# Kernel tuning notes

Hardware: AMD Instinct MI355X
Metric: run time of the kernel (lower is better)

The kernel has to match this reference:

```python
import jax, jax.numpy as jnp
import numpy as np

B, C, H, W = 16, 512, 32, 32
NUM_GROUPS = 32
EPS = 1e-5


def setup_inputs() -> dict:
    key = jax.random.key(0)
    ks = jax.random.split(key, 7)
    x = jax.random.normal(ks[0], (B, C, H, W), dtype=jnp.float32)
    gamma = jnp.ones((C,), dtype=jnp.float32)
    beta = jnp.zeros((C,), dtype=jnp.float32)
    # project_in: Conv2d(C, 3C, 1) -> weight [3C, C], bias [3C]
    w_in = jax.random.normal(ks[1], (3 * C, C), dtype=jnp.float32) / np.sqrt(C)
    b_in = jnp.zeros((3 * C,), dtype=jnp.float32)
    # project_out: Conv2d(C, C, 1) with init_scale=0.0 -> zero-init in original;
    # use small random weights so gradients/outputs are non-trivial for testing.
    w_out = jax.random.normal(ks[2], (C, C), dtype=jnp.float32) / np.sqrt(C)
    b_out = jnp.zeros((C,), dtype=jnp.float32)
    return {"x": x, "gamma": gamma, "beta": beta, "w_in": w_in, "b_in": b_in,
            "w_out": w_out, "b_out": b_out}


def group_norm(x, gamma, beta):
    b, c, h, w = x.shape
    xg = x.reshape(b, NUM_GROUPS, c // NUM_GROUPS, h, w)
    mean = xg.mean(axis=(2, 3, 4), keepdims=True)
    var = xg.var(axis=(2, 3, 4), keepdims=True)
    xn = ((xg - mean) * jax.lax.rsqrt(var + EPS)).reshape(b, c, h, w)
    return xn * gamma[None, :, None, None] + beta[None, :, None, None]


def reference(x, gamma, beta, w_in, b_in, w_out, b_out):
    skip = x  # in_channels == out_channels -> Identity skip
    xn = group_norm(x, gamma, beta)
    # 1x1 conv == channel matmul
    qkv = jnp.einsum('oc,bchw->bohw', w_in, xn) + b_in[None, :, None, None]
    q, k, v = jnp.split(qkv, 3, axis=1)  # each [B, C, H, W]
    cm = q.shape[1]
    # [B, H, W, H*W] scores
    scores = jnp.einsum('bchw,bcHW->bhwHW', q, k).reshape(B, H, W, H * W)
    attn = jax.nn.softmax(scores / jnp.sqrt(jnp.float32(cm)), axis=-1)
    attn = attn.reshape(B, H, W, H, W)
    out = jnp.einsum('bhwHW,bcHW->bchw', attn, v)
    out = jnp.einsum('oc,bchw->bohw', w_out, out) + b_out[None, :, None, None]
    return out + skip
```

## Files before the change

### kernel.cpp

```cpp
#include <hip/hip_runtime.h>
#include <hip/hip_bf16.h>
#include <cstdint>
#include <cstddef>

#define HW   1024
#define NC   512
#define NB   16
#define EPSV 1e-5f

typedef __hip_bfloat16 bf16;
typedef __attribute__((ext_vector_type(8))) __bf16 bf16x8;
typedef __attribute__((ext_vector_type(4))) float f32x4;

__device__ __forceinline__ void gload16(const void* g, void* l) {
  __builtin_amdgcn_global_load_lds(
      (const __attribute__((address_space(1))) uint32_t*)g,
      (__attribute__((address_space(3))) uint32_t*)l, 16, 0, 0);
}

__global__ __launch_bounds__(256) void cvt_w_kernel(
    const float* __restrict__ wi, const float* __restrict__ wo,
    bf16* __restrict__ wib, char* __restrict__ wobf) {
  int i = blockIdx.x * 256 + threadIdx.x;
  if (i < 196608) {
    float4 v = ((const float4*)wi)[i];
    union { bf16 h[4]; uint2 u; } p;
    p.h[0] = __float2bfloat16(v.x); p.h[1] = __float2bfloat16(v.y);
    p.h[2] = __float2bfloat16(v.z); p.h[3] = __float2bfloat16(v.w);
    *(uint2*)&wib[(size_t)i * 4] = p.u;
  } else {
    int j = i - 196608;
    float4 v = ((const float4*)wo)[j];
    int elem = j * 4;
    int co = elem >> 9, c = elem & 511;
    union { bf16 h[4]; uint2 u; } p;
    p.h[0] = __float2bfloat16(v.x); p.h[1] = __float2bfloat16(v.y);
    p.h[2] = __float2bfloat16(v.z); p.h[3] = __float2bfloat16(v.w);
    int chh = co >> 4, col_ = co & 15, kc = c >> 5, cc = c & 31;
    *(uint2*)(wobf + (((chh * 16 + kc) << 10) + col_ * 64 + cc * 2)) = p.u;
  }
}

__global__ __launch_bounds__(256) void gn_kernel(
    const float* __restrict__ x, const float* __restrict__ gamma,
    const float* __restrict__ beta, bf16* __restrict__ xn) {
  int blk = blockIdx.x;
  int b = blk >> 5, g = blk & 31;
  size_t base = ((size_t)(b * NC + g * 16)) * HW;
  const float4* src4 = (const float4*)(x + base);
  int t = threadIdx.x;
  float s = 0.f, ss = 0.f;
  float4 v[16];
#pragma unroll
  for (int i = 0; i < 16; ++i) {
    v[i] = src4[t + i * 256];
    s  += v[i].x + v[i].y + v[i].z + v[i].w;
    ss += v[i].x * v[i].x + v[i].y * v[i].y + v[i].z * v[i].z + v[i].w * v[i].w;
  }
  __shared__ float red[256];
  red[t] = s; __syncthreads();
  for (int o = 128; o > 0; o >>= 1) { if (t < o) red[t] += red[t + o]; __syncthreads(); }
  float mean = red[0] * (1.f / 16384.f);
  __syncthreads();
  red[t] = ss; __syncthreads();
  for (int o = 128; o > 0; o >>= 1) { if (t < o) red[t] += red[t + o]; __syncthreads(); }
  float var = red[0] * (1.f / 16384.f) - mean * mean;
  float rstd = rsqrtf(var + EPSV);

  __shared__ bf16 sm[16][1032];
#pragma unroll
  for (int i = 0; i < 16; ++i) {
    int idx = t + i * 256;
    int c = idx >> 8;
    int hw4 = (idx & 255) * 4;
    float gm = gamma[g * 16 + c], bt = beta[g * 16 + c];
    union { bf16 h[4]; uint2 u; } p;
    p.h[0] = __float2bfloat16((v[i].x - mean) * rstd * gm + bt);
    p.h[1] = __float2bfloat16((v[i].y - mean) * rstd * gm + bt);
    p.h[2] = __float2bfloat16((v[i].z - mean) * rstd * gm + bt);
    p.h[3] = __float2bfloat16((v[i].w - mean) * rstd * gm + bt);
    *(uint2*)&sm[c][hw4] = p.u;
  }
  __syncthreads();
  bf16* dst = xn + (size_t)b * HW * NC + g * 16;
#pragma unroll
  for (int it = 0; it < 8; ++it) {
    int u = it * 256 + t;
    int hw = u >> 1;
    int c8 = (u & 1) * 8;
    union { bf16 h[8]; uint4 q; } p;
#pragma unroll
    for (int j = 0; j < 8; ++j) p.h[j] = sm[c8 + j][hw];
    *(uint4*)&dst[(size_t)hw * NC + c8] = p.q;
  }
}

__global__ __launch_bounds__(256) void qkv_gemm(
    const bf16* __restrict__ wib, const bf16* __restrict__ xn,
    const float* __restrict__ bias,
    bf16* __restrict__ qtok, char* __restrict__ kfrag, char* __restrict__ vfrag) {
  __shared__ bf16 sT[2][128][32];
  int z = blockIdx.z;
  const bf16* Bb = xn + (size_t)z * (512 * 1024);
  int n0 = blockIdx.x * 128, m0 = blockIdx.y * 128;
  int t = threadIdx.x;
  int l = t & 63, w = t >> 6;
  int wm = w >> 1, wn = w & 1;

  int srow = t >> 2;
  int scol = (t & 3) * 8;

  f32x4 acc[4][4] = {};

  const bf16* ga0 = wib + (size_t)(m0 + srow) * 512 + scol;
  const bf16* gb0 = Bb + (size_t)(n0 + srow) * 512 + scol;

  for (int k0 = 0; k0 < 512; k0 += 32) {
    gload16(ga0 + k0, &sT[0][srow][scol]);
    gload16(ga0 + (size_t)64 * 512 + k0, &sT[0][64 + srow][scol]);
    gload16(gb0 + k0, &sT[1][srow][scol]);
    gload16(gb0 + (size_t)64 * 512 + k0, &sT[1][64 + srow][scol]);
    __syncthreads();
    bf16x8 af[4], bfr[4];
    int kc = (l >> 4) * 8;
    int ra = wm * 64 + (l & 15);
    int rb = wn * 64 + (l & 15);
#pragma unroll
    for (int i = 0; i < 4; ++i) {
      af[i]  = *(const bf16x8*)&sT[0][ra + i * 16][kc];
      bfr[i] = *(const bf16x8*)&sT[1][rb + i * 16][kc];
    }
#pragma unroll
    for (int i = 0; i < 4; ++i)
#pragma unroll
      for (int j = 0; j < 4; ++j)
        acc[i][j] = __builtin_amdgcn_mfma_f32_16x16x32_bf16(af[i], bfr[j], acc[i][j], 0, 0, 0);
    __syncthreads();
  }

  int rbase = (l >> 4) * 4;
#pragma unroll
  for (int i = 0; i < 4; ++i) {
    int row = m0 + wm * 64 + i * 16 + rbase;
    float4 bv = *(const float4*)&bias[row];
    float bb[4] = {bv.x, bv.y, bv.z, bv.w};
#pragma unroll
    for (int j = 0; j < 4; ++j) {
      int col = n0 + wn * 64 + j * 16 + (l & 15);
      if (m0 < 512) {
        bf16* C = qtok + (size_t)z * 524288;
        union { bf16 h[4]; uint2 u; } p;
#pragma unroll
        for (int r = 0; r < 4; ++r) p.h[r] = __float2bfloat16(acc[i][j][r] + bb[r]);
        *(uint2*)&C[(size_t)col * 512 + row] = p.u;
      } else if (m0 < 1024) {
        char* C = kfrag + (size_t)z * 1048576;
        int rk = row - 512;
        int jflat = col >> 4, j_lo = col & 15;
        int kw = rk >> 5, cc = rk & 31;
        union { bf16 h[4]; uint2 u; } p;
#pragma unroll
        for (int r = 0; r < 4; ++r) p.h[r] = __float2bfloat16(acc[i][j][r] + bb[r]);
        *(uint2*)(C + (((size_t)(jflat * 16 + kw)) << 10) + j_lo * 64 + cc * 2) = p.u;
      } else {
        char* C = vfrag + (size_t)z * 1048576;
        int rv = row - 1024;
        int tile = col >> 7, jj = col & 127;
        int ks = jj >> 5, jc = jj & 31;
#pragma unroll
        for (int r = 0; r < 4; ++r) {
          int ch = rv + r;
          int chh = ch >> 4, chl = ch & 15;
          *(bf16*)(C + (((tile * 32 + chh) * 4 + ks) << 10)
                     + chl * 64 + jc * 2) = __float2bfloat16(acc[i][j][r] + bb[r]);
        }
      }
    }
  }
}

__global__ __launch_bounds__(512, 1) void flash_kernel(
    const bf16* __restrict__ qtok, const bf16* __restrict__ kfrag,
    const bf16* __restrict__ vfrag, const bf16* __restrict__ wfrag,
    const float* __restrict__ b_out, const float* __restrict__ x,
    float* __restrict__ out) {
  __shared__ char lds[98304];
  char* Qs = lds;
  char* Ps = lds + 65536;
  float* redl = (float*)(lds + 65536);

  int id = blockIdx.x;
  int xcd = id & 7, rest = id >> 3;
  int q = rest & 15, bh = rest >> 4;
  int b = xcd + bh * 8;
  int i0 = q * 64;

  const char* qC = (const char*)qtok + (size_t)b * 1048576;
  const char* kC = (const char*)kfrag + (size_t)b * 1048576;
  const char* vC = (const char*)vfrag + (size_t)b * 1048576;
  const char* wC = (const char*)wfrag;

  int t = threadIdx.x, l = t & 63, w = t >> 6;
  int l15 = l & 15, lq = l >> 4;
  int fofs = l15 * 64 + lq * 16;
  int chb = w * 64;

#pragma unroll
  for (int it = 0; it < 8; ++it) {
    int A = it * 8192 + t * 16;
    int ih2 = A >> 14, ks = (A >> 10) & 15, ilo = (A >> 6) & 15, cb = A & 63;
    gload16(qC + (size_t)(i0 + ih2 * 16 + ilo) * 1024 + ks * 64 + cb, Qs + A);
  }

  float lacc[4] = {0.f, 0.f, 0.f, 0.f};
  f32x4 o[4][4] = {};
  const float scl = 0.044194173824159216f;

  __syncthreads();

  for (int tile = 0; tile < 4; ++tile) {
    bf16x8 vfA[4][4];
#pragma unroll
    for (int js = 0; js < 4; ++js)
#pragma unroll
      for (int mi = 0; mi < 4; ++mi) {
        int f = tile * 8 + js;
        vfA[js][mi] = *(const bf16x8*)(vC
            + (((size_t)(((f >> 2) * 32 + (w * 4 + mi)) * 4 + (f & 3))) << 10) + fofs);
      }
    f32x4 s0[4] = {}, s1[4] = {};
#pragma unroll
    for (int kw = 0; kw < 16; ++kw) {
      int jf0 = tile * 16 + w * 2;
      bf16x8 kf0 = *(const bf16x8*)(kC + (((size_t)(jf0 * 16 + kw)) << 10) + fofs);
      bf16x8 kf1 = *(const bf16x8*)(kC + (((size_t)((jf0 + 1) * 16 + kw)) << 10) + fofs);
#pragma unroll
      for (int ni = 0; ni < 4; ++ni) {
        bf16x8 qf = *(const bf16x8*)(Qs + ni * 16384 + kw * 1024 + fofs);
        s0[ni] = __builtin_amdgcn_mfma_f32_16x16x32_bf16(kf0, qf, s0[ni], 0, 0, 0);
        s1[ni] = __builtin_amdgcn_mfma_f32_16x16x32_bf16(kf1, qf, s1[ni], 0, 0, 0);
      }
    }
#pragma unroll
    for (int ni = 0; ni < 4; ++ni) {
#pragma unroll
      for (int jg = 0; jg < 2; ++jg) {
        const f32x4& sv = jg ? s1[ni] : s0[ni];
        float p0 = __expf(sv[0] * scl);
        float p1 = __expf(sv[1] * scl);
        float p2 = __expf(sv[2] * scl);
        float p3 = __expf(sv[3] * scl);
        lacc[ni] += p0 + p1 + p2 + p3;
        union { bf16 h[4]; uint64_t u; } pk;
        pk.h[0] = __float2bfloat16(p0); pk.h[1] = __float2bfloat16(p1);
        pk.h[2] = __float2bfloat16(p2); pk.h[3] = __float2bfloat16(p3);
        *(uint64_t*)(Ps + ni * 8192 + w * 1024 + l15 * 64 + jg * 32 + lq * 8) = pk.u;
      }
    }
    __syncthreads();
    bf16x8 vfB[4][4];
#pragma unroll
    for (int js = 0; js < 4; ++js)
#pragma unroll
      for (int mi = 0; mi < 4; ++mi) {
        int f = tile * 8 + 4 + js;
        vfB[js][mi] = *(const bf16x8*)(vC
            + (((size_t)(((f >> 2) * 32 + (w * 4 + mi)) * 4 + (f & 3))) << 10) + fofs);
      }
#pragma unroll
    for (int js = 0; js < 4; ++js)
#pragma unroll
      for (int ni = 0; ni < 4; ++ni) {
        bf16x8 pf = *(const bf16x8*)(Ps + ni * 8192 + js * 1024 + fofs);
#pragma unroll
        for (int mi = 0; mi < 4; ++mi)
          o[mi][ni] = __builtin_amdgcn_mfma_f32_16x16x32_bf16(vfA[js][mi], pf, o[mi][ni], 0, 0, 0);
      }
#pragma unroll
    for (int js = 0; js < 4; ++js)
#pragma unroll
      for (int ni = 0; ni < 4; ++ni) {
        bf16x8 pf = *(const bf16x8*)(Ps + ni * 8192 + (4 + js) * 1024 + fofs);
#pragma unroll
        for (int mi = 0; mi < 4; ++mi)
          o[mi][ni] = __builtin_amdgcn_mfma_f32_16x16x32_bf16(vfB[js][mi], pf, o[mi][ni], 0, 0, 0);
      }
    __syncthreads();
  }

#pragma unroll
  for (int ni = 0; ni < 4; ++ni) {
    float v = lacc[ni];
    v += __shfl_xor(v, 16);
    v += __shfl_xor(v, 32);
    if (l < 16) redl[w * 64 + ni * 16 + l] = v;
  }
  __syncthreads();
  float linv[4];
#pragma unroll
  for (int ni = 0; ni < 4; ++ni) {
    int i = ni * 16 + l15;
    float v = redl[i];
#pragma unroll
    for (int w2 = 1; w2 < 8; ++w2) v += redl[w2 * 64 + i];
    linv[ni] = 1.f / v;
  }
#pragma unroll
  for (int mi = 0; mi < 4; ++mi)
#pragma unroll
    for (int ni = 0; ni < 4; ++ni) {
      union { bf16 h[4]; uint64_t u; } pk;
#pragma unroll
      for (int r = 0; r < 4; ++r)
        pk.h[r] = __float2bfloat16(o[mi][ni][r] * linv[ni]);
      int dst = ni * 16384 + (w * 2 + (mi >> 1)) * 1024 + l15 * 64
              + (mi & 1) * 32 + lq * 8;
      *(uint64_t*)(Qs + dst) = pk.u;
    }
  __syncthreads();

  f32x4 acc2[4][4] = {};
#pragma unroll
  for (int kc = 0; kc < 16; ++kc) {
    bf16x8 wf[4];
#pragma unroll
    for (int mi = 0; mi < 4; ++mi)
      wf[mi] = *(const bf16x8*)(wC + (((size_t)(w * 4 + mi) * 16 + kc) << 10) + fofs);
#pragma unroll
    for (int ni = 0; ni < 4; ++ni) {
      bf16x8 pf = *(const bf16x8*)(Qs + ni * 16384 + kc * 1024 + fofs);
#pragma unroll
      for (int mi = 0; mi < 4; ++mi)
        acc2[mi][ni] = __builtin_amdgcn_mfma_f32_16x16x32_bf16(wf[mi], pf, acc2[mi][ni], 0, 0, 0);
    }
  }

  const float* xb = x + (size_t)b * 524288;
  float* ob = out + (size_t)b * 524288;
#pragma unroll
  for (int mi = 0; mi < 4; ++mi) {
    int cbase = chb + mi * 16 + lq * 4;
    float4 bv = *(const float4*)&b_out[cbase];
    float bb[4] = {bv.x, bv.y, bv.z, bv.w};
#pragma unroll
    for (int ni = 0; ni < 4; ++ni) {
      int i = i0 + ni * 16 + l15;
#pragma unroll
      for (int r = 0; r < 4; ++r) {
        size_t off = (size_t)(cbase + r) * 1024 + i;
        ob[off] = acc2[mi][ni][r] + bb[r] + xb[off];
      }
    }
  }
}

extern "C" void kernel_launch(void* const* d_in, const int* in_sizes, int n_in,
                              void* d_out, int out_size, void* d_ws, size_t ws_size,
                              hipStream_t stream) {
  const float* x     = (const float*)d_in[0];
  const float* gamma = (const float*)d_in[1];
  const float* beta  = (const float*)d_in[2];
  const float* w_in  = (const float*)d_in[3];
  const float* b_in  = (const float*)d_in[4];
  const float* w_out = (const float*)d_in[5];
  const float* b_out = (const float*)d_in[6];
  float* out = (float*)d_out;

  char* w = (char*)d_ws;
  bf16* xn    = (bf16*)w;
  bf16* qtok  = (bf16*)(w + ((size_t)16 << 20));
  bf16* kfrag = (bf16*)(w + ((size_t)32 << 20));
  bf16* vfrag = (bf16*)(w + ((size_t)48 << 20));
  bf16* wib   = (bf16*)(w + ((size_t)64 << 20));
  char* wobf  = (char*)(w + ((size_t)64 << 20) + ((size_t)3 << 19));

  cvt_w_kernel<<<1024, 256, 0, stream>>>(w_in, w_out, wib, wobf);
  gn_kernel<<<NB * 32, 256, 0, stream>>>(x, gamma, beta, xn);

  qkv_gemm<<<dim3(8, 12, NB), 256, 0, stream>>>(
      wib, xn, b_in, qtok, (char*)kfrag, (char*)vfrag);

  flash_kernel<<<256, 512, 0, stream>>>(qtok, kfrag, vfrag, (const bf16*)wobf,
                                        b_out, x, out);
}
```

Before: 128.5 us.

## Double flash block to 16 waves with larger key tiles and pipelined V loads

```diff
diff --git a/kernel.cpp b/kernel.cpp
--- a/kernel.cpp
+++ b/kernel.cpp
@@ -179,12 +179,12 @@
   }
 }
 
-__global__ __launch_bounds__(512, 1) void flash_kernel(
+__global__ __launch_bounds__(1024, 4) void flash_kernel(
     const bf16* __restrict__ qtok, const bf16* __restrict__ kfrag,
     const bf16* __restrict__ vfrag, const bf16* __restrict__ wfrag,
     const float* __restrict__ b_out, const float* __restrict__ x,
     float* __restrict__ out) {
-  __shared__ char lds[98304];
+  __shared__ char lds[131072];
   char* Qs = lds;
   char* Ps = lds + 65536;
   float* redl = (float*)(lds + 65536);
@@ -203,35 +203,25 @@
   int t = threadIdx.x, l = t & 63, w = t >> 6;
   int l15 = l & 15, lq = l >> 4;
   int fofs = l15 * 64 + lq * 16;
-  int chb = w * 64;
-
-#pragma unroll
-  for (int it = 0; it < 8; ++it) {
-    int A = it * 8192 + t * 16;
+
+#pragma unroll
+  for (int it = 0; it < 4; ++it) {
+    int A = it * 16384 + t * 16;
     int ih2 = A >> 14, ks = (A >> 10) & 15, ilo = (A >> 6) & 15, cb = A & 63;
     gload16(qC + (size_t)(i0 + ih2 * 16 + ilo) * 1024 + ks * 64 + cb, Qs + A);
   }
 
   float lacc[4] = {0.f, 0.f, 0.f, 0.f};
-  f32x4 o[4][4] = {};
+  f32x4 o[2][4] = {};
   const float scl = 0.044194173824159216f;
 
   __syncthreads();
 
-  for (int tile = 0; tile < 4; ++tile) {
-    bf16x8 vfA[4][4];
-#pragma unroll
-    for (int js = 0; js < 4; ++js)
-#pragma unroll
-      for (int mi = 0; mi < 4; ++mi) {
-        int f = tile * 8 + js;
-        vfA[js][mi] = *(const bf16x8*)(vC
-            + (((size_t)(((f >> 2) * 32 + (w * 4 + mi)) * 4 + (f & 3))) << 10) + fofs);
-      }
+  for (int tile = 0; tile < 2; ++tile) {
     f32x4 s0[4] = {}, s1[4] = {};
 #pragma unroll
     for (int kw = 0; kw < 16; ++kw) {
-      int jf0 = tile * 16 + w * 2;
+      int jf0 = tile * 32 + w * 2;
       bf16x8 kf0 = *(const bf16x8*)(kC + (((size_t)(jf0 * 16 + kw)) << 10) + fofs);
       bf16x8 kf1 = *(const bf16x8*)(kC + (((size_t)((jf0 + 1) * 16 + kw)) << 10) + fofs);
 #pragma unroll
@@ -254,37 +244,46 @@
         union { bf16 h[4]; uint64_t u; } pk;
         pk.h[0] = __float2bfloat16(p0); pk.h[1] = __float2bfloat16(p1);
         pk.h[2] = __float2bfloat16(p2); pk.h[3] = __float2bfloat16(p3);
-        *(uint64_t*)(Ps + ni * 8192 + w * 1024 + l15 * 64 + jg * 32 + lq * 8) = pk.u;
+        *(uint64_t*)(Ps + ni * 16384 + w * 1024 + l15 * 64 + jg * 32 + lq * 8) = pk.u;
       }
     }
     __syncthreads();
-    bf16x8 vfB[4][4];
-#pragma unroll
-    for (int js = 0; js < 4; ++js)
-#pragma unroll
-      for (int mi = 0; mi < 4; ++mi) {
-        int f = tile * 8 + 4 + js;
-        vfB[js][mi] = *(const bf16x8*)(vC
-            + (((size_t)(((f >> 2) * 32 + (w * 4 + mi)) * 4 + (f & 3))) << 10) + fofs);
-      }
-#pragma unroll
-    for (int js = 0; js < 4; ++js)
-#pragma unroll
-      for (int ni = 0; ni < 4; ++ni) {
-        bf16x8 pf = *(const bf16x8*)(Ps + ni * 8192 + js * 1024 + fofs);
-#pragma unroll
-        for (int mi = 0; mi < 4; ++mi)
-          o[mi][ni] = __builtin_amdgcn_mfma_f32_16x16x32_bf16(vfA[js][mi], pf, o[mi][ni], 0, 0, 0);
-      }
-#pragma unroll
-    for (int js = 0; js < 4; ++js)
-#pragma unroll
-      for (int ni = 0; ni < 4; ++ni) {
-        bf16x8 pf = *(const bf16x8*)(Ps + ni * 8192 + (4 + js) * 1024 + fofs);
-#pragma unroll
-        for (int mi = 0; mi < 4; ++mi)
-          o[mi][ni] = __builtin_amdgcn_mfma_f32_16x16x32_bf16(vfB[js][mi], pf, o[mi][ni], 0, 0, 0);
-      }
+    bf16x8 vfA[4][2], vfB[4][2];
+#pragma unroll
+    for (int ss = 0; ss < 4; ++ss)
+#pragma unroll
+      for (int mi = 0; mi < 2; ++mi) {
+        int f = tile * 16 + ss;
+        vfA[ss][mi] = *(const bf16x8*)(vC
+            + (((size_t)(((f >> 2) * 32 + (w * 2 + mi)) * 4 + (f & 3))) << 10) + fofs);
+      }
+#pragma unroll
+    for (int qtr = 0; qtr < 4; ++qtr) {
+      if (qtr < 3) {
+#pragma unroll
+        for (int ss = 0; ss < 4; ++ss)
+#pragma unroll
+          for (int mi = 0; mi < 2; ++mi) {
+            int f = tile * 16 + (qtr + 1) * 4 + ss;
+            bf16x8 v = *(const bf16x8*)(vC
+                + (((size_t)(((f >> 2) * 32 + (w * 2 + mi)) * 4 + (f & 3))) << 10) + fofs);
+            if (qtr & 1) vfA[ss][mi] = v; else vfB[ss][mi] = v;
+          }
+      }
+#pragma unroll
+      for (int ss = 0; ss < 4; ++ss) {
+        int slot = qtr * 4 + ss;
+#pragma unroll
+        for (int ni = 0; ni < 4; ++ni) {
+          bf16x8 pf = *(const bf16x8*)(Ps + ni * 16384 + slot * 1024 + fofs);
+#pragma unroll
+          for (int mi = 0; mi < 2; ++mi) {
+            bf16x8 vv = (qtr & 1) ? vfB[ss][mi] : vfA[ss][mi];
+            o[mi][ni] = __builtin_amdgcn_mfma_f32_16x16x32_bf16(vv, pf, o[mi][ni], 0, 0, 0);
+          }
+        }
+      }
+    }
     __syncthreads();
   }
 
@@ -302,35 +301,34 @@
     int i = ni * 16 + l15;
     float v = redl[i];
 #pragma unroll
-    for (int w2 = 1; w2 < 8; ++w2) v += redl[w2 * 64 + i];
+    for (int w2 = 1; w2 < 16; ++w2) v += redl[w2 * 64 + i];
     linv[ni] = 1.f / v;
   }
 #pragma unroll
-  for (int mi = 0; mi < 4; ++mi)
+  for (int mi = 0; mi < 2; ++mi)
 #pragma unroll
     for (int ni = 0; ni < 4; ++ni) {
       union { bf16 h[4]; uint64_t u; } pk;
 #pragma unroll
       for (int r = 0; r < 4; ++r)
         pk.h[r] = __float2bfloat16(o[mi][ni][r] * linv[ni]);
-      int dst = ni * 16384 + (w * 2 + (mi >> 1)) * 1024 + l15 * 64
-              + (mi & 1) * 32 + lq * 8;
+      int dst = ni * 16384 + w * 1024 + l15 * 64 + mi * 32 + lq * 8;
       *(uint64_t*)(Qs + dst) = pk.u;
     }
   __syncthreads();
 
-  f32x4 acc2[4][4] = {};
+  f32x4 acc2[2][4] = {};
 #pragma unroll
   for (int kc = 0; kc < 16; ++kc) {
-    bf16x8 wf[4];
-#pragma unroll
-    for (int mi = 0; mi < 4; ++mi)
-      wf[mi] = *(const bf16x8*)(wC + (((size_t)(w * 4 + mi) * 16 + kc) << 10) + fofs);
+    bf16x8 wf[2];
+#pragma unroll
+    for (int mi = 0; mi < 2; ++mi)
+      wf[mi] = *(const bf16x8*)(wC + (((size_t)((w * 2 + mi) * 16 + kc)) << 10) + fofs);
 #pragma unroll
     for (int ni = 0; ni < 4; ++ni) {
       bf16x8 pf = *(const bf16x8*)(Qs + ni * 16384 + kc * 1024 + fofs);
 #pragma unroll
-      for (int mi = 0; mi < 4; ++mi)
+      for (int mi = 0; mi < 2; ++mi)
         acc2[mi][ni] = __builtin_amdgcn_mfma_f32_16x16x32_bf16(wf[mi], pf, acc2[mi][ni], 0, 0, 0);
     }
   }
@@ -338,8 +336,8 @@
   const float* xb = x + (size_t)b * 524288;
   float* ob = out + (size_t)b * 524288;
 #pragma unroll
-  for (int mi = 0; mi < 4; ++mi) {
-    int cbase = chb + mi * 16 + lq * 4;
+  for (int mi = 0; mi < 2; ++mi) {
+    int cbase = w * 32 + mi * 16 + lq * 4;
     float4 bv = *(const float4*)&b_out[cbase];
     float bb[4] = {bv.x, bv.y, bv.z, bv.w};
 #pragma unroll
@@ -380,6 +378,6 @@
   qkv_gemm<<<dim3(8, 12, NB), 256, 0, stream>>>(
       wib, xn, b_in, qtok, (char*)kfrag, (char*)vfrag);
 
-  flash_kernel<<<256, 512, 0, stream>>>(qtok, kfrag, vfrag, (const bf16*)wobf,
-                                        b_out, x, out);
-}
+  flash_kernel<<<256, 1024, 0, stream>>>(qtok, kfrag, vfrag, (const bf16*)wobf,
+                                         b_out, x, out);
+}
```

After: 128.6 us. Within noise of the previous version (+0.0%).
